# Performance work log

Hardware: AMD Instinct MI355X
Metric: run time of the kernel (lower is better)

Reference implementation:

```python
import jax, jax.numpy as jnp
import numpy as np

C1 = 1e-4
C2 = 9e-4
WIN = 25
FOCAL_GAMMA = 2.0
IGNORE_INDEX = 255


def focal_loss(logits, target):
    # standard focal CE: -(1-p_t)^gamma * log p_t, mean over valid pixels
    logp = jax.nn.log_softmax(logits, axis=1)            # [B,C,H,W]
    tgt = jnp.clip(target, 0, logits.shape[1] - 1)
    logp_t = jnp.take_along_axis(logp, tgt[:, None], axis=1)[:, 0]  # [B,H,W]
    pt = jnp.exp(logp_t)
    loss = -((1.0 - pt) ** FOCAL_GAMMA) * logp_t
    valid = (target != IGNORE_INDEX).astype(loss.dtype)
    return jnp.sum(loss * valid) / jnp.maximum(jnp.sum(valid), 1.0)


def iou_loss(pred, targ):
    p = pred.reshape(pred.shape[0], -1)
    t = targ.reshape(targ.shape[0], -1)
    inter = jnp.sum(p * t)
    union = p.sum() + t.sum() - inter
    return 1.0 - (inter + 0.1) / (union + 0.1)


def ssim_batch(img1, img2, win=WIN):
    B, C, H, W = img1.shape
    nh, nw = H // win, W // win

    def to_windows(x):
        x = x[:, :, : nh * win, : nw * win]
        x = x.reshape(B, C, nh, win, nw, win)
        return x.transpose(0, 2, 4, 1, 3, 5).reshape(B, nh, nw, -1)

    w1 = to_windows(img1)
    w2 = to_windows(img2)
    n = w1.shape[-1]
    m1 = jnp.mean(w1, axis=-1)
    m2 = jnp.mean(w2, axis=-1)
    d1 = w1 - m1[..., None]
    d2 = w2 - m2[..., None]
    var1 = jnp.sum(d1 * d1, axis=-1) / (n - 1)   # torch.std is unbiased
    var2 = jnp.sum(d2 * d2, axis=-1) / (n - 1)
    cov = jnp.mean(d1 * d2, axis=-1)             # batch_im_cov is biased
    c = (2 * m1 * m2 + C1) / (m1 * m1 + m2 * m2 + C1)
    s = (2 * cov + C2) / (var1 + var2 + C2)
    sim = c * s                                   # beta = gamma = 1
    # original skips a window if ANY batch element is NaN for it
    valid = ~jnp.any(jnp.isnan(sim), axis=0)      # [nh, nw]
    total = jnp.sum(jnp.where(valid[None], sim, 0.0), axis=(1, 2))  # [B]
    return total / (nh * nw + 1e-4)


def setup_inputs() -> dict:
    key = jax.random.key(0)
    k1, k2 = jax.random.split(key)
    pred = jax.random.normal(k1, (8, 21, 512, 512), dtype=jnp.float32)
    target = jax.random.randint(k2, (8, 512, 512), 0, 21, dtype=jnp.int32)
    return {"pred": pred, "target": target}


def reference(pred, target):
    num_classes = pred.shape[1]
    floss = focal_loss(pred, target)
    # onehot_softmax
    prob = jax.nn.softmax(pred, axis=1)
    tgt_c = jnp.clip(target, 0, num_classes)
    onehot = jax.nn.one_hot(tgt_c, num_classes + 1, dtype=prob.dtype)[..., :num_classes]
    onehot = jnp.transpose(onehot, (0, 3, 1, 2))  # [B,C,H,W]
    iou = iou_loss(prob, onehot)
    # ms_ssim_loss with single scale, dropping background channel
    sim = ssim_batch(prob[:, 1:], onehot[:, 1:])
    msssim = 1.0 - sim                            # [B]
    return floss + iou + msssim                   # [B]
```

## Files before the change

kernel.cpp:

```cpp
#include <hip/hip_runtime.h>


constexpr int B_ = 8, C_ = 21, H_ = 512, W_ = 512;
constexpr int WIN = 25, NH = 20, NW = 20;
constexpr int HW = H_ * W_;
constexpr int HW4 = HW / 4;
constexpr int CROP = 500;
constexpr int NBLK_MAIN = B_ * (H_ / 2);
constexpr int RP_OFF4 = NBLK_MAIN;

__device__ __forceinline__ float wave_sum(float v) {
#pragma unroll
  for (int off = 32; off > 0; off >>= 1) v += __shfl_xor(v, off, 64);
  return v;
}

template <int K, int NWAVE>
__device__ __forceinline__ void block_sum_n(float (&vals)[K], float* lds, int tid) {
  const int lane = tid & 63, wid = tid >> 6;
#pragma unroll
  for (int k = 0; k < K; ++k) {
    float v = wave_sum(vals[k]);
    if (lane == 0) lds[k * NWAVE + wid] = v;
  }
  __syncthreads();
  if (tid == 0) {
#pragma unroll
    for (int k = 0; k < K; ++k) {
      float s = 0.f;
#pragma unroll
      for (int w = 0; w < NWAVE; ++w) s += lds[k * NWAVE + w];
      vals[k] = s;
    }
  }
}

__global__ __launch_bounds__(256) void main_kernel(
    const float* __restrict__ pred, const int* __restrict__ target,
    float* __restrict__ ws) {
  const int tid = threadIdx.x;
  const int tile = (blockIdx.x & 7) * (NBLK_MAIN / 8) + (blockIdx.x >> 3);
  const int b = tile >> 8;
  const int row0 = (tile & 255) << 1;
  const int rsub = tid >> 7;
  const int row = row0 + rsub;
  const int cgrp = tid & 127;
  const int col = cgrp << 2;

  const int4 t4 =
      reinterpret_cast<const int4*>(target)[(size_t)b * HW4 + row * 128 + cgrp];

  const float4* __restrict__ base =
      reinterpret_cast<const float4*>(pred) + (size_t)b * C_ * HW4 + row * 128 + cgrp;

  float4 v[C_];
#pragma unroll
  for (int c = 0; c < C_; ++c) v[c] = base[(size_t)c * HW4];

  const int tcx = min(max(t4.x, 0), C_ - 1);
  const int tcy = min(max(t4.y, 0), C_ - 1);
  const int tcz = min(max(t4.z, 0), C_ - 1);
  const int tcw = min(max(t4.w, 0), C_ - 1);

  float4 S0 = {0,0,0,0}, S1 = {0,0,0,0}, Q1 = {0,0,0,0};
  float4 ET = {0,0,0,0}, XT = {0,0,0,0};
#pragma unroll
  for (int c = 0; c < C_; ++c) {
#define COMP(CMP, TC)                                     \
    {                                                     \
      const float xv = v[c].CMP;                          \
      const float e = __expf(xv);                         \
      S0.CMP += e;                                        \
      if (c >= 1) { S1.CMP += e; Q1.CMP += e * e; }       \
      if (c == (TC)) { ET.CMP = e; XT.CMP = xv; }         \
    }
    COMP(x, tcx) COMP(y, tcy) COMP(z, tcz) COMP(w, tcw)
#undef COMP
  }

  float focal = 0, valid = 0, inter = 0, ohc = 0;
  const int wjA = col / 25;
  float accA0 = 0, accA1 = 0, accA2 = 0, accA3 = 0;
  float accB0 = 0, accB1 = 0, accB2 = 0, accB3 = 0;
#define EPI(CMP, K)                                                     \
  {                                                                     \
    const int t = t4.CMP;                                               \
    const float inv = 1.0f / S0.CMP;                                    \
    const float pt_ = ET.CMP * inv;                                     \
    if (t != 255) {                                                     \
      const float logp = XT.CMP - __logf(S0.CMP);                       \
      const float om = 1.0f - pt_;                                      \
      focal += om * om * (-logp);                                       \
      valid += 1.0f;                                                    \
    }                                                                   \
    if (t <= 20) { inter += pt_; ohc += 1.0f; }                         \
    const float s1v = S1.CMP * inv;                                     \
    const float s1qv = Q1.CMP * inv * inv;                              \
    const bool insim = (t >= 1 && t <= 20);                             \
    const float s12v = insim ? pt_ : 0.0f;                              \
    const float s2v = insim ? 1.0f : 0.0f;                              \
    if (row < CROP && (col + K) < CROP) {                               \
      if ((col + K) / 25 == wjA) {                                      \
        accA0 += s1v; accA1 += s1qv; accA2 += s12v; accA3 += s2v;       \
      } else {                                                          \
        accB0 += s1v; accB1 += s1qv; accB2 += s12v; accB3 += s2v;       \
      }                                                                 \
    }                                                                   \
  }
  EPI(x, 0) EPI(y, 1) EPI(z, 2) EPI(w, 3)
#undef EPI

  __shared__ float bins[2][NW][4];
  if (tid < 2 * NW * 4) reinterpret_cast<float*>(bins)[tid] = 0.f;
  __syncthreads();
  if (row < CROP) {
    if (wjA < NW) {
      atomicAdd(&bins[rsub][wjA][0], accA0);
      atomicAdd(&bins[rsub][wjA][1], accA1);
      atomicAdd(&bins[rsub][wjA][2], accA2);
      atomicAdd(&bins[rsub][wjA][3], accA3);
    }
    const int wjB = (col + 3) / 25;
    if (wjB != wjA && wjB < NW) {
      atomicAdd(&bins[rsub][wjB][0], accB0);
      atomicAdd(&bins[rsub][wjB][1], accB1);
      atomicAdd(&bins[rsub][wjB][2], accB2);
      atomicAdd(&bins[rsub][wjB][3], accB3);
    }
  }
  __syncthreads();
  if (tid < 2 * NW) {
    const int r = tid / NW, wj = tid - (tid / NW) * NW;
    if (row0 + r < CROP) {
      reinterpret_cast<float4*>(ws)[RP_OFF4 + ((size_t)(b * 512 + row0 + r) * NW + wj)] =
          make_float4(bins[r][wj][0], bins[r][wj][1], bins[r][wj][2], bins[r][wj][3]);
    }
  }

  float vals[4] = {focal, valid, inter, ohc};
  __shared__ float lds[4 * 4];
  block_sum_n<4, 4>(vals, lds, tid);
  if (tid == 0) {
    reinterpret_cast<float4*>(ws)[blockIdx.x] =
        make_float4(vals[0], vals[1], vals[2], vals[3]);
  }
}

__global__ __launch_bounds__(512) void reduce_kernel(
    const float* __restrict__ ws, float* __restrict__ out) {
  const int b = blockIdx.x;
  const int tid = threadIdx.x;
  const float4* __restrict__ part = reinterpret_cast<const float4*>(ws);

  float4 a = {0, 0, 0, 0};
  for (int i = tid; i < NBLK_MAIN; i += 512) {
    const float4 p = part[i];
    a.x += p.x; a.y += p.y; a.z += p.z; a.w += p.w;
  }

  float sim = 0.f;
  if (tid < NH * NW) {
    const int wi = tid / NW, wj = tid - (tid / NW) * NW;
    const float4* __restrict__ rp =
        part + RP_OFF4 + ((size_t)(b * 512 + wi * WIN) * NW + wj);
    float S1 = 0, S1q = 0, S12 = 0, S2 = 0;
#pragma unroll
    for (int r = 0; r < WIN; ++r) {
      const float4 s = rp[(size_t)r * NW];
      S1 += s.x; S1q += s.y; S12 += s.z; S2 += s.w;
    }
    const double n = (double)(C_ - 1) * WIN * WIN;
    const double m1 = S1 / n, m2 = S2 / n;
    const double var1 = (S1q - (double)S1 * S1 / n) / (n - 1.0);
    const double var2 = (S2 - (double)S2 * S2 / n) / (n - 1.0);
    const double cov = (S12 - (double)S1 * S2 / n) / n;
    const double cterm = (2.0 * m1 * m2 + 0.0001) / (m1 * m1 + m2 * m2 + 0.0001);
    const double sterm = (2.0 * cov + 0.0009) / (var1 + var2 + 0.0009);
    sim = (float)(cterm * sterm);
  }

  float vals[5] = {a.x, a.y, a.z, a.w, sim};
  __shared__ float lds[5 * 8];
  block_sum_n<5, 8>(vals, lds, tid);
  if (tid == 0) {
    const float floss = vals[0] / fmaxf(vals[1], 1.0f);
    const float inter = vals[2];
    const float psum = (float)((size_t)B_ * HW);
    const float uni = psum + vals[3] - inter;
    const float iou = 1.0f - (inter + 0.1f) / (uni + 0.1f);
    out[b] = floss + iou + (1.0f - vals[4] / (400.0f + 0.0001f));
  }
}

extern "C" void kernel_launch(void* const* d_in, const int* in_sizes, int n_in,
                              void* d_out, int out_size, void* d_ws, size_t ws_size,
                              hipStream_t stream) {
  (void)in_sizes; (void)n_in; (void)out_size; (void)ws_size;
  const float* pred = (const float*)d_in[0];
  const int* target = (const int*)d_in[1];
  float* out = (float*)d_out;
  float* ws = (float*)d_ws;

  main_kernel<<<NBLK_MAIN, 256, 0, stream>>>(pred, target, ws);
  reduce_kernel<<<B_, 512, 0, stream>>>(ws, out);
}
```

Measured before the change: 48.06 us.

## Stage class loads through LDS with async global_load_lds triple buffering

Replaces the 21 direct float4 register loads per thread with asynchronous global-to-LDS DMA loads (global_load_lds, 16 bytes) into a 3-deep staging buffer of 4 channels each, with manual vmcnt/lgkmcnt waits to overlap loading with the exp/accumulate work. The aim is to cut register pressure from holding all 21 float4s and keep memory requests in flight while computing. It adds 48KB of LDS per block, which may lower occupancy, and depends on hand-written waitcnt sequencing that is fragile if the compiler reorders or issues other memory ops.

Result: slower. 51.99 us (+8.2%).

```diff
diff --git a/kernel.cpp b/kernel.cpp
--- a/kernel.cpp
+++ b/kernel.cpp
@@ -8,6 +8,9 @@
 constexpr int CROP = 500;
 constexpr int NBLK_MAIN = B_ * (H_ / 2);
 constexpr int RP_OFF4 = NBLK_MAIN;
+
+#define VMCNT(n) asm volatile("s_waitcnt vmcnt(" #n ")" ::: "memory")
+#define LGKM0    asm volatile("s_waitcnt lgkmcnt(0)" ::: "memory")
 
 __device__ __forceinline__ float wave_sum(float v) {
 #pragma unroll
@@ -46,16 +49,25 @@
   const int row = row0 + rsub;
   const int cgrp = tid & 127;
   const int col = cgrp << 2;
+  const int wv = tid >> 6, ln = tid & 63;
+
+  __shared__ float stage[3][4][1024];
 
   const int4 t4 =
       reinterpret_cast<const int4*>(target)[(size_t)b * HW4 + row * 128 + cgrp];
 
-  const float4* __restrict__ base =
+  const float4* __restrict__ gthr =
       reinterpret_cast<const float4*>(pred) + (size_t)b * C_ * HW4 + row * 128 + cgrp;
 
-  float4 v[C_];
-#pragma unroll
-  for (int c = 0; c < C_; ++c) v[c] = base[(size_t)c * HW4];
+#define DMA4(g)                                                           \
+  { _Pragma("unroll") for (int cc = 0; cc < 4; ++cc) {                    \
+      __builtin_amdgcn_global_load_lds(                                   \
+          (const void*)(gthr + (size_t)((g) * 4 + cc) * HW4),             \
+          (void*)(&stage[(g) % 3][cc][wv << 8]), 16, 0, 0);               \
+    } }
+#define DMA1(ch, bf)                                                      \
+  __builtin_amdgcn_global_load_lds((const void*)(gthr + (size_t)(ch) * HW4), \
+                                   (void*)(&stage[bf][0][wv << 8]), 16, 0, 0);
 
   const int tcx = min(max(t4.x, 0), C_ - 1);
   const int tcy = min(max(t4.y, 0), C_ - 1);
@@ -64,19 +76,47 @@
 
   float4 S0 = {0,0,0,0}, S1 = {0,0,0,0}, Q1 = {0,0,0,0};
   float4 ET = {0,0,0,0}, XT = {0,0,0,0};
-#pragma unroll
-  for (int c = 0; c < C_; ++c) {
-#define COMP(CMP, TC)                                     \
-    {                                                     \
-      const float xv = v[c].CMP;                          \
-      const float e = __expf(xv);                         \
-      S0.CMP += e;                                        \
-      if (c >= 1) { S1.CMP += e; Q1.CMP += e * e; }       \
-      if (c == (TC)) { ET.CMP = e; XT.CMP = xv; }         \
-    }
-    COMP(x, tcx) COMP(y, tcy) COMP(z, tcz) COMP(w, tcw)
-#undef COMP
-  }
+
+#define COMP1(XV, CMP, c)                               \
+  {                                                     \
+    const float xv = (XV);                              \
+    const float e = __expf(xv);                         \
+    S0.CMP += e;                                        \
+    if ((c) >= 1) { S1.CMP += e; Q1.CMP += e * e; }     \
+    if ((c) == tc##CMP) { ET.CMP = e; XT.CMP = xv; }    \
+  }
+#define COMPV(VV, c) \
+  COMP1((VV).x, x, c) COMP1((VV).y, y, c) COMP1((VV).z, z, c) COMP1((VV).w, w, c)
+#define CONSUME4(g)                                                        \
+  { float4 q0 = reinterpret_cast<const float4*>(&stage[(g)%3][0][wv<<8])[ln]; \
+    float4 q1 = reinterpret_cast<const float4*>(&stage[(g)%3][1][wv<<8])[ln]; \
+    float4 q2 = reinterpret_cast<const float4*>(&stage[(g)%3][2][wv<<8])[ln]; \
+    float4 q3 = reinterpret_cast<const float4*>(&stage[(g)%3][3][wv<<8])[ln]; \
+    COMPV(q0, (g)*4+0) COMPV(q1, (g)*4+1) COMPV(q2, (g)*4+2) COMPV(q3, (g)*4+3) }
+
+  DMA4(0) DMA4(1) DMA4(2)
+  VMCNT(8);
+  CONSUME4(0) LGKM0;
+  DMA4(3)
+  VMCNT(8);
+  CONSUME4(1) LGKM0;
+  DMA4(4)
+  VMCNT(8);
+  CONSUME4(2) LGKM0;
+  DMA1(20, 2)
+  VMCNT(5);
+  CONSUME4(3) LGKM0;
+  VMCNT(1);
+  CONSUME4(4) LGKM0;
+  VMCNT(0);
+  { float4 q0 = reinterpret_cast<const float4*>(&stage[2][0][wv<<8])[ln];
+    COMPV(q0, 20) }
+
+#undef CONSUME4
+#undef COMPV
+#undef COMP1
+#undef DMA4
+#undef DMA1
 
   float focal = 0, valid = 0, inter = 0, ohc = 0;
   const int wjA = col / 25;
```
